# Kernel tuning notes

Measured on AMD Instinct MI355X. Metric: run time of the kernel, lower is better.

## Reference

```python
import jax, jax.numpy as jnp
import numpy as np


def silu(x):
    return x * jax.nn.sigmoid(x)


def conv1x1(x, w, s, b, act):
    # x: [B,Ci,H,W], w: [Co,Ci]; BN folded into per-channel scale s / bias b
    y = jnp.einsum('oi,bihw->bohw', w, x) * s[None, :, None, None] + b[None, :, None, None]
    return silu(y) if act else y


def dwconv3x3(x, w, s, b):
    # depthwise 3x3, groups=C, padding SAME (autopad=1); w: [C,1,3,3]
    y = jax.lax.conv_general_dilated(
        x, w, window_strides=(1, 1), padding=[(1, 1), (1, 1)],
        dimension_numbers=('NCHW', 'OIHW', 'NCHW'),
        feature_group_count=x.shape[1])
    return y * s[None, :, None, None] + b[None, :, None, None]


def attention(x, qkv_w, qkv_s, qkv_b, pe_w, pe_s, pe_b, proj_w, proj_s, proj_b,
              num_heads=4, key_dim=32, head_dim=64):
    B, C, H, W = x.shape
    N = H * W
    scale = key_dim ** -0.5
    qkv = conv1x1(x, qkv_w, qkv_s, qkv_b, act=False)          # [B, C+2*nh*kd, H, W]
    qkv = qkv.reshape(B, num_heads, key_dim * 2 + head_dim, N)
    q = qkv[:, :, :key_dim]                                    # [B,nh,kd,N]
    k = qkv[:, :, key_dim:2 * key_dim]                         # [B,nh,kd,N]
    v = qkv[:, :, 2 * key_dim:]                                # [B,nh,hd,N]
    attn = jnp.einsum('bhdi,bhdj->bhij', q, k) * scale         # [B,nh,N,N]
    attn = jax.nn.softmax(attn, axis=-1)
    out = jnp.einsum('bhdj,bhij->bhdi', v, attn)               # [B,nh,hd,N]
    out = out.reshape(B, C, H, W) + dwconv3x3(v.reshape(B, C, H, W), pe_w, pe_s, pe_b)
    return conv1x1(out, proj_w, proj_s, proj_b, act=False)


def setup_inputs() -> dict:
    key = jax.random.key(0)
    ks = jax.random.split(key, 32)
    B, C1, H, W = 4, 512, 48, 48
    c = C1 // 2  # 256
    h = c + 2 * 32 * 4  # 512
    d = {'x': jax.random.normal(ks[0], (B, C1, H, W), jnp.float32)}
    def w(i, shape):
        return jax.random.normal(ks[i], shape, jnp.float32) * 0.05
    def s(i, n):
        return jax.random.uniform(ks[i], (n,), jnp.float32, 0.5, 1.5)
    def b(i, n):
        return jax.random.normal(ks[i], (n,), jnp.float32) * 0.05
    d['cv1_w'], d['cv1_s'], d['cv1_b'] = w(1, (2 * c, C1)), s(2, 2 * c), b(3, 2 * c)
    d['qkv_w'], d['qkv_s'], d['qkv_b'] = w(4, (h, c)), s(5, h), b(6, h)
    d['pe_w'], d['pe_s'], d['pe_b'] = w(7, (c, 1, 3, 3)), s(8, c), b(9, c)
    d['proj_w'], d['proj_s'], d['proj_b'] = w(10, (c, c)), s(11, c), b(12, c)
    d['ffn1_w'], d['ffn1_s'], d['ffn1_b'] = w(13, (2 * c, c)), s(14, 2 * c), b(15, 2 * c)
    d['ffn2_w'], d['ffn2_s'], d['ffn2_b'] = w(16, (c, 2 * c)), s(17, c), b(18, c)
    d['cv2_w'], d['cv2_s'], d['cv2_b'] = w(19, (C1, 2 * c)), s(20, C1), b(21, C1)
    return d


def reference(x, cv1_w, cv1_s, cv1_b, qkv_w, qkv_s, qkv_b, pe_w, pe_s, pe_b,
              proj_w, proj_s, proj_b, ffn1_w, ffn1_s, ffn1_b, ffn2_w, ffn2_s, ffn2_b,
              cv2_w, cv2_s, cv2_b):
    c = cv1_w.shape[0] // 2  # hidden channels (256)
    ab = conv1x1(x, cv1_w, cv1_s, cv1_b, act=True)
    a, bb = ab[:, :c], ab[:, c:]
    bb = bb + attention(bb, qkv_w, qkv_s, qkv_b, pe_w, pe_s, pe_b,
                        proj_w, proj_s, proj_b)
    f = conv1x1(bb, ffn1_w, ffn1_s, ffn1_b, act=True)
    bb = bb + conv1x1(f, ffn2_w, ffn2_s, ffn2_b, act=False)
    return conv1x1(jnp.concatenate([a, bb], axis=1), cv2_w, cv2_s, cv2_b, act=True)
```

## Files before the change

### kernel.cpp

```cpp
#include <hip/hip_runtime.h>
#include <math.h>

#define N_SP 2304
#define HW 48

typedef unsigned short u16;
typedef short s8v  __attribute__((ext_vector_type(8)));
typedef short s4v  __attribute__((ext_vector_type(4)));
typedef u16   u16x8 __attribute__((ext_vector_type(8)));
typedef float f32x4 __attribute__((ext_vector_type(4)));
typedef unsigned u32x4 __attribute__((ext_vector_type(4)));

__device__ __forceinline__ short f2bf(float x) {
    unsigned u = __float_as_uint(x);
    u += 0x7FFFu + ((u >> 16) & 1u);
    return (short)(u >> 16);
}
__device__ __forceinline__ float bf2f(u16 u) {
    return __uint_as_float((unsigned)u << 16);
}
__device__ __forceinline__ float fexp2(float x) { return __builtin_amdgcn_exp2f(x); }
__device__ __forceinline__ float frcp(float x)  { return __builtin_amdgcn_rcpf(x); }
__device__ __forceinline__ float fsilu(float v) {
    return v * frcp(1.f + fexp2(-1.4426950408889634f * v));
}
__device__ __forceinline__ unsigned cvtpk(float lo, float hi) {
    unsigned r;
    asm("v_cvt_pk_bf16_f32 %0, %1, %2" : "=v"(r) : "v"(lo), "v"(hi));
    return r;
}
__device__ __forceinline__ void gload16(const void* g, void* l) {
    __builtin_amdgcn_global_load_lds(
        (const __attribute__((address_space(1))) void*)g,
        (__attribute__((address_space(3))) void*)l, 16, 0, 0);
}
__device__ __forceinline__ void bar_lgkm() {
    asm volatile("s_waitcnt lgkmcnt(0)" ::: "memory");
    __builtin_amdgcn_s_barrier();
}

__global__ __launch_bounds__(256) void prep(
    const float* __restrict__ X, u16* __restrict__ XT,
    const float* __restrict__ s0, const float* __restrict__ s1,
    const float* __restrict__ s2, const float* __restrict__ s3,
    const float* __restrict__ s4, const float* __restrict__ s5,
    u16* __restrict__ d0, u16* __restrict__ d1, u16* __restrict__ d2,
    u16* __restrict__ d3, u16* __restrict__ d4, u16* __restrict__ d5)
{
    __shared__ float tile[64][65];
    const int t = threadIdx.x;
    if (blockIdx.x < 960) {
        int id = blockIdx.x * 256 + t;
        const int c0 = 65536, c1 = c0 + 32768, c2 = c1 + 16384,
                  c3 = c2 + 32768, c4 = c3 + 32768, c5 = c4 + 65536;
        if (id >= c5) return;
        const float* s; u16* d; int off;
        if      (id < c0) { s = s0; d = d0; off = id; }
        else if (id < c1) { s = s1; d = d1; off = id - c0; }
        else if (id < c2) { s = s2; d = d2; off = id - c1; }
        else if (id < c3) { s = s3; d = d3; off = id - c2; }
        else if (id < c4) { s = s4; d = d4; off = id - c3; }
        else              { s = s5; d = d5; off = id - c4; }
        float4 v = ((const float4*)s)[off];
        s4v p; p[0] = f2bf(v.x); p[1] = f2bf(v.y); p[2] = f2bf(v.z); p[3] = f2bf(v.w);
        ((s4v*)d)[off] = p;
        return;
    }
    const int bid = blockIdx.x - 960;
    const int n0 = (bid % 36) * 64, c0 = ((bid / 36) & 7) * 64, b = bid / 288;
    const float* src = X + (long)b * 512 * N_SP;
    u16* dst = XT + (long)b * N_SP * 512;
    #pragma unroll
    for (int it = 0; it < 16; ++it) {
        int id = t + 256 * it;
        int cl = id >> 6, nl = id & 63;
        tile[cl][nl] = src[(long)(c0 + cl) * N_SP + n0 + nl];
    }
    __syncthreads();
    #pragma unroll
    for (int it = 0; it < 16; ++it) {
        int id = t + 256 * it;
        int nl = id >> 6, cl = id & 63;
        dst[(long)(n0 + nl) * 512 + c0 + cl] = f2bf(tile[cl][nl]);
    }
}

template <int OMODE>
__device__ __forceinline__ void gemm_epilogue(
    float y[4], int nb, int nib, int o, int b_blk, int Mtot,
    const u16* Res, int sR, void* OutP, u16* OutT, int sO)
{
    if (Res) {
        #pragma unroll
        for (int r = 0; r < 4; ++r)
            y[r] += bf2f(Res[(long)(nb + r) * sR + o]);
    }
    if (OMODE == 0) {
        u16* O = (u16*)OutP;
        #pragma unroll
        for (int r = 0; r < 4; ++r)
            O[(long)(nb + r) * sO + o] = (u16)f2bf(y[r]);
    } else if (OMODE == 1 || OMODE == 3) {
        u16* O = (u16*)OutP + (long)b_blk * Mtot * N_SP + (long)o * N_SP + nib;
        s4v pk;
        #pragma unroll
        for (int r = 0; r < 4; ++r) pk[r] = f2bf(y[r]);
        *(s4v*)O = pk;
        if (OMODE == 3) {
            #pragma unroll
            for (int r = 0; r < 4; ++r)
                OutT[(long)(nb + r) * 512 + o] = (u16)f2bf(y[r]);
        }
    } else {
        float* O = (float*)OutP + (long)b_blk * Mtot * N_SP + (long)o * N_SP + nib;
        *(float4*)O = make_float4(y[0], y[1], y[2], y[3]);
    }
}

template <int NO, int OMODE>
__global__ __launch_bounds__(256) void mfma_gemm(
    const u16* __restrict__ A1, const u16* __restrict__ A2, int K1,
    int sA1, int sA2, int K,
    const u16* __restrict__ W,
    const float* __restrict__ S, const float* __restrict__ Bi,
    const u16* __restrict__ Res, int sR,
    void* __restrict__ OutP, u16* __restrict__ OutT, int sO, int Mtot,
    int act)
{
    __shared__ u16 Al[3][64][64];
    __shared__ u16 Bl[3][64][64];
    const int t  = threadIdx.x;
    const int p = blockIdx.x;
    const int cx = p & 7, q = p >> 3;
    const int n0 = (cx * 18 + q / NO) * 64;
    const int o0 = (q % NO) * 64;
    const int lane = t & 63, w = t >> 6;
    const int wn = (w & 1) * 32, wo = (w >> 1) * 32;
    const int li = lane & 15, g = lane >> 4;

    const int b_blk = n0 / N_SP;
    const int n_in0 = n0 - b_blk * N_SP;

    f32x4 acc[2][2];
    #pragma unroll
    for (int fm = 0; fm < 2; ++fm)
        #pragma unroll
        for (int fn = 0; fn < 2; ++fn) acc[fm][fn] = f32x4{0.f, 0.f, 0.f, 0.f};

    auto issue = [&](int buf, int k0) {
        #pragma unroll
        for (int qq = 0; qq < 2; ++qq) {
            int c = t + qq * 256;
            int row = c >> 3;
            int col = ((c & 7) ^ (row & 7)) * 8;
            int kk = k0 + col;
            const u16* ga = (kk < K1) ? (A1 + (long)(n0 + row) * sA1 + kk)
                                      : (A2 + (long)(n0 + row) * sA2 + (kk - K1));
            gload16(ga, (u16*)Al[buf] + (qq * 256 + w * 64) * 8);
            gload16(W + (long)(o0 + row) * K + k0 + col,
                    (u16*)Bl[buf] + (qq * 256 + w * 64) * 8);
        }
    };

    const int NK = K >> 6;
    issue(0, 0);
    if (NK > 1) issue(1, 64);

    for (int ks = 0; ks < NK; ++ks) {
        if (ks + 1 < NK) asm volatile("s_waitcnt vmcnt(4)" ::: "memory");
        else             asm volatile("s_waitcnt vmcnt(0)" ::: "memory");
        __builtin_amdgcn_s_barrier();
        if (ks + 2 < NK) issue((ks + 2) % 3, (ks + 2) << 6);
        const int cur = ks % 3;
        #pragma unroll
        for (int k2 = 0; k2 < 2; ++k2) {
            s8v af[2], bfv[2];
            #pragma unroll
            for (int fm = 0; fm < 2; ++fm) {
                int row = wn + fm * 16 + li;
                af[fm] = *(const s8v*)&Al[cur][row][((g + 4 * k2) ^ (li & 7)) * 8];
            }
            #pragma unroll
            for (int fn = 0; fn < 2; ++fn) {
                int row = wo + fn * 16 + li;
                bfv[fn] = *(const s8v*)&Bl[cur][row][((g + 4 * k2) ^ (li & 7)) * 8];
            }
            #pragma unroll
            for (int fm = 0; fm < 2; ++fm)
                #pragma unroll
                for (int fn = 0; fn < 2; ++fn)
                    acc[fm][fn] = __builtin_amdgcn_mfma_f32_16x16x32_bf16(
                        af[fm], bfv[fn], acc[fm][fn], 0, 0, 0);
        }
    }

    #pragma unroll
    for (int fn = 0; fn < 2; ++fn) {
        const int o = o0 + wo + fn * 16 + li;
        const float sc2 = S[o], bi = Bi[o];
        #pragma unroll
        for (int fm = 0; fm < 2; ++fm) {
            const int nb  = n0 + wn + fm * 16 + 4 * g;
            const int nib = n_in0 + wn + fm * 16 + 4 * g;
            float y[4];
            #pragma unroll
            for (int r = 0; r < 4; ++r) {
                float v = acc[fm][fn][r] * sc2 + bi;
                if (act) v = fsilu(v);
                y[r] = v;
            }
            gemm_epilogue<OMODE>(y, nb, nib, o, b_blk, Mtot, Res, sR, OutP, OutT, sO);
        }
    }
}

template <int NO, int OMODE>
__global__ __launch_bounds__(256) void mfma_gemm_big(
    const u16* __restrict__ A1, const u16* __restrict__ A2, int K1,
    int sA1, int sA2, int K,
    const u16* __restrict__ W,
    const float* __restrict__ S, const float* __restrict__ Bi,
    const u16* __restrict__ Res, int sR,
    void* __restrict__ OutP, u16* __restrict__ OutT, int sO, int Mtot,
    int act)
{
    __shared__ u16 Al[2][128][64];
    __shared__ u16 Bl[2][64][64];
    const int t  = threadIdx.x;
    const int p = blockIdx.x;
    const int cx = p & 7, q = p >> 3;
    const int n0 = (cx * 9 + q / NO) * 128;
    const int o0 = (q % NO) * 64;
    const int lane = t & 63, w = t >> 6;
    const int wn = (w & 1) * 64, wo = (w >> 1) * 32;
    const int li = lane & 15, g = lane >> 4;

    const int b_blk = n0 / N_SP;
    const int n_in0 = n0 - b_blk * N_SP;

    f32x4 acc[4][2];
    #pragma unroll
    for (int fm = 0; fm < 4; ++fm)
        #pragma unroll
        for (int fn = 0; fn < 2; ++fn) acc[fm][fn] = f32x4{0.f, 0.f, 0.f, 0.f};

    auto issue = [&](int buf, int k0) {
        #pragma unroll
        for (int qq = 0; qq < 4; ++qq) {
            int c = t + qq * 256;
            int row = c >> 3;
            int col = ((c & 7) ^ (row & 7)) * 8;
            int kk = k0 + col;
            const u16* ga = (kk < K1) ? (A1 + (long)(n0 + row) * sA1 + kk)
                                      : (A2 + (long)(n0 + row) * sA2 + (kk - K1));
            gload16(ga, (u16*)Al[buf] + (qq * 256 + w * 64) * 8);
        }
        #pragma unroll
        for (int qq = 0; qq < 2; ++qq) {
            int c = t + qq * 256;
            int row = c >> 3;
            int col = ((c & 7) ^ (row & 7)) * 8;
            gload16(W + (long)(o0 + row) * K + k0 + col,
                    (u16*)Bl[buf] + (qq * 256 + w * 64) * 8);
        }
    };

    const int NK = K >> 6;
    issue(0, 0);
    asm volatile("s_waitcnt vmcnt(0)" ::: "memory");
    __builtin_amdgcn_s_barrier();

    int cur = 0;
    for (int ks = 0; ks < NK; ++ks) {
        if (ks + 1 < NK) issue(cur ^ 1, (ks + 1) << 6);
        #pragma unroll
        for (int k2 = 0; k2 < 2; ++k2) {
            s8v af[4], bfv[2];
            #pragma unroll
            for (int fm = 0; fm < 4; ++fm) {
                int row = wn + fm * 16 + li;
                af[fm] = *(const s8v*)&Al[cur][row][((g + 4 * k2) ^ (li & 7)) * 8];
            }
            #pragma unroll
            for (int fn = 0; fn < 2; ++fn) {
                int row = wo + fn * 16 + li;
                bfv[fn] = *(const s8v*)&Bl[cur][row][((g + 4 * k2) ^ (li & 7)) * 8];
            }
            #pragma unroll
            for (int fm = 0; fm < 4; ++fm)
                #pragma unroll
                for (int fn = 0; fn < 2; ++fn)
                    acc[fm][fn] = __builtin_amdgcn_mfma_f32_16x16x32_bf16(
                        af[fm], bfv[fn], acc[fm][fn], 0, 0, 0);
        }
        if (ks + 1 < NK) {
            asm volatile("s_waitcnt vmcnt(0)" ::: "memory");
            __builtin_amdgcn_s_barrier();
        }
        cur ^= 1;
    }

    #pragma unroll
    for (int fn = 0; fn < 2; ++fn) {
        const int o = o0 + wo + fn * 16 + li;
        const float sc2 = S[o], bi = Bi[o];
        #pragma unroll
        for (int fm = 0; fm < 4; ++fm) {
            const int nb  = n0 + wn + fm * 16 + 4 * g;
            const int nib = n_in0 + wn + fm * 16 + 4 * g;
            float y[4];
            #pragma unroll
            for (int r = 0; r < 4; ++r) {
                float v = acc[fm][fn][r] * sc2 + bi;
                if (act) v = fsilu(v);
                y[r] = v;
            }
            gemm_epilogue<OMODE>(y, nb, nib, o, b_blk, Mtot, Res, sR, OutP, OutT, sO);
        }
    }
}

__global__ __launch_bounds__(256) void attn_mfma(const u16* __restrict__ qkv,
    const u16* __restrict__ qkvT,
    u16* __restrict__ Opart, float* __restrict__ mpart, float* __restrict__ lpart)
{
    const int N = N_SP;
    __shared__ u16 Klds[2][64][40];
    __shared__ u16 Vlds[2][64][72];

    const int p = blockIdx.x;
    const int cx = p & 7, q = p >> 3;
    const int i0 = (q % 18) * 128;
    const int bhz = cx + 8 * (q / 18);
    const int bh = bhz & 15, z = bhz >> 4;
    const int b = bh >> 2, h = bh & 3;
    const int t = threadIdx.x;
    const int w = t >> 6;
    const int lane = t & 63;
    const int li = lane & 15;
    const int g  = lane >> 4;
    const float qscale = 0.17677669529663687f * 1.4426950408889634f;

    const u16* qp  = qkv  + ((long)b * 512 + (long)h * 128) * N;
    const u16* vp  = qp + 64L * N;
    const u16* qTp = qkvT + (long)b * N * 512 + h * 128;

    const int ia = i0 + w * 16 + li;
    const int ib = ia + 64;

    s8v qf[2];
    {
        s8v qa = *(const s8v*)(qTp + (long)ia * 512 + 8 * g);
        s8v qb = *(const s8v*)(qTp + (long)ib * 512 + 8 * g);
        #pragma unroll
        for (int r = 0; r < 8; ++r) {
            qf[0][r] = f2bf(bf2f((u16)qa[r]) * qscale);
            qf[1][r] = f2bf(bf2f((u16)qb[r]) * qscale);
        }
    }

    f32x4 oacc[2][4];
    #pragma unroll
    for (int q2 = 0; q2 < 2; ++q2)
        #pragma unroll
        for (int dt = 0; dt < 4; ++dt) oacc[q2][dt] = f32x4{0.f, 0.f, 0.f, 0.f};
    float m_run[2] = {-1e30f, -1e30f}, l_run[2] = {0.f, 0.f};

    const int kj2 = t & 63;
    const int kd  = (t >> 6) * 8;
    const int vd  = t >> 2;
    const int vjb = (t & 3) * 16;

    const int jbase = z * 576;
    u16x8 kr, vr0, vr1;
    auto ldregs = [&](int j0) {
        kr  = *(const u16x8*)(qTp + (long)(j0 + kj2) * 512 + 32 + kd);
        vr0 = *(const u16x8*)(vp + (long)vd * N + j0 + vjb);
        vr1 = *(const u16x8*)(vp + (long)vd * N + j0 + vjb + 8);
    };

    ldregs(jbase);
    *(u16x8*)&Klds[0][kj2][kd]     = kr;
    *(u16x8*)&Vlds[0][vd][vjb]     = vr0;
    *(u16x8*)&Vlds[0][vd][vjb + 8] = vr1;
    ldregs(jbase + 64);
    bar_lgkm();

    int cur = 0;
    for (int it = 0; it < 9; ++it) {
        if (it + 1 < 9) {
            *(u16x8*)&Klds[cur ^ 1][kj2][kd]     = kr;
            *(u16x8*)&Vlds[cur ^ 1][vd][vjb]     = vr0;
            *(u16x8*)&Vlds[cur ^ 1][vd][vjb + 8] = vr1;
            if (it + 2 < 9) ldregs(jbase + (it + 2) * 64);
        }

        f32x4 sacc[2][4];
        __builtin_amdgcn_s_setprio(1);
        #pragma unroll
        for (int js = 0; js < 4; ++js) {
            s8v kf = *(const s8v*)&Klds[cur][js * 16 + li][8 * g];
            f32x4 zz = f32x4{0.f, 0.f, 0.f, 0.f};
            sacc[0][js] = __builtin_amdgcn_mfma_f32_16x16x32_bf16(kf, qf[0], zz, 0, 0, 0);
            sacc[1][js] = __builtin_amdgcn_mfma_f32_16x16x32_bf16(kf, qf[1], zz, 0, 0, 0);
        }
        __builtin_amdgcn_s_setprio(0);

        #pragma unroll
        for (int q2 = 0; q2 < 2; ++q2) {
            float tm = -1e30f;
            #pragma unroll
            for (int js = 0; js < 4; ++js)
                #pragma unroll
                for (int r = 0; r < 4; ++r) tm = fmaxf(tm, sacc[q2][js][r]);
            tm = fmaxf(tm, __shfl_xor(tm, 16, 64));
            tm = fmaxf(tm, __shfl_xor(tm, 32, 64));
            if (__any(tm > m_run[q2] + 8.f)) {
                float mnew = fmaxf(m_run[q2], tm);
                float scl  = fexp2(m_run[q2] - mnew);
                l_run[q2] *= scl;
                #pragma unroll
                for (int dt = 0; dt < 4; ++dt) oacc[q2][dt] *= scl;
                m_run[q2] = mnew;
            }
            float ts = 0.f;
            #pragma unroll
            for (int js = 0; js < 4; ++js)
                #pragma unroll
                for (int r = 0; r < 4; ++r) {
                    float pv = fexp2(sacc[q2][js][r] - m_run[q2]);
                    sacc[q2][js][r] = pv;
                    ts += pv;
                }
            ts += __shfl_xor(ts, 16, 64);
            ts += __shfl_xor(ts, 32, 64);
            l_run[q2] += ts;
        }

        __builtin_amdgcn_s_setprio(1);
        #pragma unroll
        for (int ks = 0; ks < 2; ++ks) {
            s8v pf[2];
            #pragma unroll
            for (int q2 = 0; q2 < 2; ++q2) {
                u32x4 pw;
                pw[0] = cvtpk(sacc[q2][2 * ks][0],     sacc[q2][2 * ks][1]);
                pw[1] = cvtpk(sacc[q2][2 * ks][2],     sacc[q2][2 * ks][3]);
                pw[2] = cvtpk(sacc[q2][2 * ks + 1][0], sacc[q2][2 * ks + 1][1]);
                pw[3] = cvtpk(sacc[q2][2 * ks + 1][2], sacc[q2][2 * ks + 1][3]);
                pf[q2] = __builtin_bit_cast(s8v, pw);
            }
            #pragma unroll
            for (int dt = 0; dt < 4; ++dt) {
                int d = dt * 16 + li;
                s4v lo = *(const s4v*)&Vlds[cur][d][32 * ks + 4 * g];
                s4v hi = *(const s4v*)&Vlds[cur][d][32 * ks + 16 + 4 * g];
                s8v vf = __builtin_shufflevector(lo, hi, 0, 1, 2, 3, 4, 5, 6, 7);
                oacc[0][dt] = __builtin_amdgcn_mfma_f32_16x16x32_bf16(vf, pf[0], oacc[0][dt], 0, 0, 0);
                oacc[1][dt] = __builtin_amdgcn_mfma_f32_16x16x32_bf16(vf, pf[1], oacc[1][dt], 0, 0, 0);
            }
        }
        __builtin_amdgcn_s_setprio(0);

        if (it + 1 < 9) bar_lgkm();
        cur ^= 1;
    }

    const long cb = (long)(z * 16 + bh);
    #pragma unroll
    for (int q2 = 0; q2 < 2; ++q2) {
        const int i = q2 ? ib : ia;
        #pragma unroll
        for (int dt = 0; dt < 4; ++dt)
            #pragma unroll
            for (int r = 0; r < 4; ++r)
                Opart[(cb * 64 + dt * 16 + 4 * g + r) * N + i] = (u16)f2bf(oacc[q2][dt][r]);
        if (g == 0) {
            mpart[cb * N + i] = m_run[q2];
            lpart[cb * N + i] = l_run[q2];
        }
    }
}

__global__ __launch_bounds__(256) void attn_combine(
    const u16* __restrict__ Opart, const float* __restrict__ mpart,
    const float* __restrict__ lpart, const u16* __restrict__ qkvT,
    const float* __restrict__ pw, const float* __restrict__ ps,
    const float* __restrict__ pb, u16* __restrict__ attnT)
{
    const int N = N_SP;
    const int i0 = blockIdx.x * 64;
    const int bh = blockIdx.y;
    const int b = bh >> 2, h = bh & 3;
    const int t = threadIdx.x;
    const int il = t & 63, dq = t >> 6;
    const int d0 = dq * 16;
    const int i = i0 + il;

    float mm[4], ll[4];
    #pragma unroll
    for (int c = 0; c < 4; ++c) {
        mm[c] = mpart[((long)(c * 16 + bh)) * N + i];
        ll[c] = lpart[((long)(c * 16 + bh)) * N + i];
    }
    float ms = fmaxf(fmaxf(mm[0], mm[1]), fmaxf(mm[2], mm[3]));
    float wc[4], lsum = 0.f;
    #pragma unroll
    for (int c = 0; c < 4; ++c) {
        wc[c] = fexp2(mm[c] - ms);
        lsum += wc[c] * ll[c];
    }
    float inv = frcp(lsum);

    const int y = i / HW, x = i - (i / HW) * HW;
    const u16* vT = qkvT + (long)b * N * 512 + h * 128 + 64 + d0;
    float pe[16];
    #pragma unroll
    for (int dd = 0; dd < 16; ++dd) pe[dd] = 0.f;
    #pragma unroll
    for (int dy = -1; dy <= 1; ++dy) {
        int yy = y + dy;
        if (yy < 0 || yy >= HW) continue;
        #pragma unroll
        for (int dx = -1; dx <= 1; ++dx) {
            int xx = x + dx;
            if (xx < 0 || xx >= HW) continue;
            const int k = (dy + 1) * 3 + (dx + 1);
            const u16* pvt = vT + (long)(yy * HW + xx) * 512;
            u16x8 a0 = *(const u16x8*)pvt;
            u16x8 a1 = *(const u16x8*)(pvt + 8);
            #pragma unroll
            for (int dd = 0; dd < 8; ++dd) {
                pe[dd]     += pw[(h * 64 + d0 + dd) * 9 + k]     * bf2f((u16)a0[dd]);
                pe[8 + dd] += pw[(h * 64 + d0 + 8 + dd) * 9 + k] * bf2f((u16)a1[dd]);
            }
        }
    }

    u16 ob[16];
    #pragma unroll
    for (int dd = 0; dd < 16; ++dd) {
        const int d = d0 + dd;
        const int cg = h * 64 + d;
        float o = 0.f;
        #pragma unroll
        for (int c = 0; c < 4; ++c)
            o += wc[c] * bf2f(Opart[((long)(c * 16 + bh) * 64 + d) * N + i]);
        o = o * inv + pe[dd] * ps[cg] + pb[cg];
        ob[dd] = (u16)f2bf(o);
    }
    u16* dst = attnT + ((long)b * N + i) * 256 + h * 64 + d0;
    *(u16x8*)dst       = *(u16x8*)&ob[0];
    *(u16x8*)(dst + 8) = *(u16x8*)&ob[8];
}

extern "C" void kernel_launch(void* const* d_in, const int* in_sizes, int n_in,
                              void* d_out, int out_size, void* d_ws, size_t ws_size,
                              hipStream_t stream)
{
    const long N = N_SP;
    const float* x      = (const float*)d_in[0];
    const float* cv1_w  = (const float*)d_in[1];
    const float* cv1_s  = (const float*)d_in[2];
    const float* cv1_b  = (const float*)d_in[3];
    const float* qkv_w  = (const float*)d_in[4];
    const float* qkv_s  = (const float*)d_in[5];
    const float* qkv_b  = (const float*)d_in[6];
    const float* pe_w   = (const float*)d_in[7];
    const float* pe_s   = (const float*)d_in[8];
    const float* pe_b   = (const float*)d_in[9];
    const float* proj_w = (const float*)d_in[10];
    const float* proj_s = (const float*)d_in[11];
    const float* proj_b = (const float*)d_in[12];
    const float* ffn1_w = (const float*)d_in[13];
    const float* ffn1_s = (const float*)d_in[14];
    const float* ffn1_b = (const float*)d_in[15];
    const float* ffn2_w = (const float*)d_in[16];
    const float* ffn2_s = (const float*)d_in[17];
    const float* ffn2_b = (const float*)d_in[18];
    const float* cv2_w  = (const float*)d_in[19];
    const float* cv2_s  = (const float*)d_in[20];
    const float* cv2_b  = (const float*)d_in[21];
    float* out = (float*)d_out;

    u16* ws = (u16*)d_ws;
    u16* xT      = ws;
    u16* abT     = xT      + 4L * N * 512;
    u16* qkvb    = abT     + 4L * N * 512;
    u16* qkvT    = qkvb    + 4L * N * 512;
    u16* attnT   = qkvT    + 4L * N * 512;
    u16* bb2T    = attnT   + 4L * N * 256;
    u16* fT      = bb2T    + 4L * N * 256;
    u16* bb3T    = fT      + 4L * N * 512;
    u16* w_cv1   = bb3T    + 4L * N * 256;
    u16* w_qkv   = w_cv1   + 512L * 512;
    u16* w_proj  = w_qkv   + 512L * 256;
    u16* w_ffn1  = w_proj  + 256L * 256;
    u16* w_ffn2  = w_ffn1  + 512L * 256;
    u16* w_cv2   = w_ffn2  + 256L * 512;
    u16* Opart   = w_cv2   + 512L * 512;
    float* mpart = (float*)(Opart + 4L * 16 * 64 * N);
    float* lpart = mpart + 4L * 16 * N;

    dim3 blk(256);
    const int BIGK = 1 << 28;

    prep<<<2112, blk, 0, stream>>>(x, xT,
        cv1_w, qkv_w, proj_w, ffn1_w, ffn2_w, cv2_w,
        w_cv1, w_qkv, w_proj, w_ffn1, w_ffn2, w_cv2);

    mfma_gemm_big<8, 0><<<576, blk, 0, stream>>>(
        xT, nullptr, BIGK, 512, 0, 512, w_cv1, cv1_s, cv1_b,
        nullptr, 0, abT, nullptr, 512, 512, 1);

    mfma_gemm_big<8, 3><<<576, blk, 0, stream>>>(
        abT + 256, nullptr, BIGK, 512, 0, 256, w_qkv, qkv_s, qkv_b,
        nullptr, 0, qkvb, qkvT, 0, 512, 0);

    attn_mfma<<<1152, blk, 0, stream>>>(qkvb, qkvT, Opart, mpart, lpart);

    attn_combine<<<dim3(36, 16), blk, 0, stream>>>(
        Opart, mpart, lpart, qkvT, pe_w, pe_s, pe_b, attnT);

    mfma_gemm<4, 0><<<576, blk, 0, stream>>>(
        attnT, nullptr, BIGK, 256, 0, 256, w_proj, proj_s, proj_b,
        abT + 256, 512, bb2T, nullptr, 256, 256, 0);

    mfma_gemm_big<8, 0><<<576, blk, 0, stream>>>(
        bb2T, nullptr, BIGK, 256, 0, 256, w_ffn1, ffn1_s, ffn1_b,
        nullptr, 0, fT, nullptr, 512, 512, 1);

    mfma_gemm<4, 0><<<576, blk, 0, stream>>>(
        fT, nullptr, BIGK, 512, 0, 512, w_ffn2, ffn2_s, ffn2_b,
        bb2T, 256, bb3T, nullptr, 256, 256, 0);

    mfma_gemm_big<8, 2><<<576, blk, 0, stream>>>(
        abT, bb3T, 256, 512, 256, 512, w_cv2, cv2_s, cv2_b,
        nullptr, 0, out, nullptr, 0, 512, 1);
}
```

Baseline: 125.6 us.

## Fuse attention combine and depthwise PE into proj GEMM kernel

Merges the split-softmax combine plus depthwise positional conv with the projection 1x1 GEMM and residual add in one kernel. Each block computes a 32-pixel x 256-channel attention tile into LDS, then runs MFMA against double-buffered proj weight slices. This removes the attnT round trip through global memory and one kernel launch. The cost is a grid of only 288 blocks with heavier per-thread register use (32 pe accumulators), which may lower occupancy and parallelism compared with the previous 576-block launches.

```diff
diff --git a/kernel.cpp b/kernel.cpp
--- a/kernel.cpp
+++ b/kernel.cpp
@@ -482,76 +482,155 @@
     }
 }
 
-__global__ __launch_bounds__(256) void attn_combine(
+__global__ __launch_bounds__(256) void combine_proj(
     const u16* __restrict__ Opart, const float* __restrict__ mpart,
     const float* __restrict__ lpart, const u16* __restrict__ qkvT,
     const float* __restrict__ pw, const float* __restrict__ ps,
-    const float* __restrict__ pb, u16* __restrict__ attnT)
+    const float* __restrict__ pb,
+    const u16* __restrict__ Wp, const float* __restrict__ S,
+    const float* __restrict__ Bi, const u16* __restrict__ abT,
+    u16* __restrict__ bb2T)
 {
     const int N = N_SP;
-    const int i0 = blockIdx.x * 64;
-    const int bh = blockIdx.y;
-    const int b = bh >> 2, h = bh & 3;
-    const int t = threadIdx.x;
-    const int il = t & 63, dq = t >> 6;
-    const int d0 = dq * 16;
-    const int i = i0 + il;
-
-    float mm[4], ll[4];
-    #pragma unroll
-    for (int c = 0; c < 4; ++c) {
-        mm[c] = mpart[((long)(c * 16 + bh)) * N + i];
-        ll[c] = lpart[((long)(c * 16 + bh)) * N + i];
-    }
-    float ms = fmaxf(fmaxf(mm[0], mm[1]), fmaxf(mm[2], mm[3]));
-    float wc[4], lsum = 0.f;
-    #pragma unroll
-    for (int c = 0; c < 4; ++c) {
-        wc[c] = fexp2(mm[c] - ms);
-        lsum += wc[c] * ll[c];
-    }
-    float inv = frcp(lsum);
-
-    const int y = i / HW, x = i - (i / HW) * HW;
-    const u16* vT = qkvT + (long)b * N * 512 + h * 128 + 64 + d0;
-    float pe[16];
-    #pragma unroll
-    for (int dd = 0; dd < 16; ++dd) pe[dd] = 0.f;
-    #pragma unroll
-    for (int dy = -1; dy <= 1; ++dy) {
-        int yy = y + dy;
-        if (yy < 0 || yy >= HW) continue;
-        #pragma unroll
-        for (int dx = -1; dx <= 1; ++dx) {
-            int xx = x + dx;
-            if (xx < 0 || xx >= HW) continue;
-            const int k = (dy + 1) * 3 + (dx + 1);
-            const u16* pvt = vT + (long)(yy * HW + xx) * 512;
-            u16x8 a0 = *(const u16x8*)pvt;
-            u16x8 a1 = *(const u16x8*)(pvt + 8);
+    __shared__ u16 At[8][32][40];
+    __shared__ u16 Wl[2][256][32];
+
+    const int bid = blockIdx.x;
+    const int i0 = (bid % 72) * 32;
+    const int b  = bid / 72;
+    const int t  = threadIdx.x;
+    const int lane = t & 63, w = t >> 6;
+    const int li = lane & 15, g = lane >> 4;
+
+    auto issueW = [&](int buf, int ks) {
+        #pragma unroll
+        for (int qq = 0; qq < 4; ++qq) {
+            int idx = qq * 256 + t;
+            int row = idx >> 2, c = idx & 3;
+            gload16(Wp + (long)row * 256 + ks * 32 + ((c ^ (row & 3)) * 8),
+                    (u16*)Wl[buf] + (qq * 256 + w * 64) * 8);
+        }
+    };
+    issueW(0, 0);
+
+    {
+        const int il  = t & 31;
+        const int grp = t >> 5;
+        const int i   = i0 + il;
+        const int h   = grp >> 1;
+        const int d0  = (grp & 1) * 32;
+        const int bh  = b * 4 + h;
+
+        float mm[4], ll[4];
+        #pragma unroll
+        for (int c = 0; c < 4; ++c) {
+            mm[c] = mpart[((long)(c * 16 + bh)) * N + i];
+            ll[c] = lpart[((long)(c * 16 + bh)) * N + i];
+        }
+        float ms = fmaxf(fmaxf(mm[0], mm[1]), fmaxf(mm[2], mm[3]));
+        float wc[4], lsum = 0.f;
+        #pragma unroll
+        for (int c = 0; c < 4; ++c) {
+            wc[c] = fexp2(mm[c] - ms);
+            lsum += wc[c] * ll[c];
+        }
+        float inv = frcp(lsum);
+
+        const int y = i / HW, x = i - (i / HW) * HW;
+        const u16* vT = qkvT + (long)b * N * 512 + h * 128 + 64 + d0;
+        float pe[32];
+        #pragma unroll
+        for (int dd = 0; dd < 32; ++dd) pe[dd] = 0.f;
+        #pragma unroll
+        for (int dy = -1; dy <= 1; ++dy) {
+            int yy = y + dy;
+            if (yy < 0 || yy >= HW) continue;
+            #pragma unroll
+            for (int dx = -1; dx <= 1; ++dx) {
+                int xx = x + dx;
+                if (xx < 0 || xx >= HW) continue;
+                const int k = (dy + 1) * 3 + (dx + 1);
+                const u16* pvt = vT + (long)(yy * HW + xx) * 512;
+                #pragma unroll
+                for (int v8 = 0; v8 < 4; ++v8) {
+                    u16x8 a = *(const u16x8*)(pvt + v8 * 8);
+                    #pragma unroll
+                    for (int dd = 0; dd < 8; ++dd)
+                        pe[v8 * 8 + dd] +=
+                            pw[(h * 64 + d0 + v8 * 8 + dd) * 9 + k] * bf2f((u16)a[dd]);
+                }
+            }
+        }
+
+        #pragma unroll
+        for (int c8 = 0; c8 < 4; ++c8) {
+            u16x8 outv;
             #pragma unroll
             for (int dd = 0; dd < 8; ++dd) {
-                pe[dd]     += pw[(h * 64 + d0 + dd) * 9 + k]     * bf2f((u16)a0[dd]);
-                pe[8 + dd] += pw[(h * 64 + d0 + 8 + dd) * 9 + k] * bf2f((u16)a1[dd]);
-            }
-        }
-    }
-
-    u16 ob[16];
-    #pragma unroll
-    for (int dd = 0; dd < 16; ++dd) {
-        const int d = d0 + dd;
-        const int cg = h * 64 + d;
-        float o = 0.f;
-        #pragma unroll
-        for (int c = 0; c < 4; ++c)
-            o += wc[c] * bf2f(Opart[((long)(c * 16 + bh) * 64 + d) * N + i]);
-        o = o * inv + pe[dd] * ps[cg] + pb[cg];
-        ob[dd] = (u16)f2bf(o);
-    }
-    u16* dst = attnT + ((long)b * N + i) * 256 + h * 64 + d0;
-    *(u16x8*)dst       = *(u16x8*)&ob[0];
-    *(u16x8*)(dst + 8) = *(u16x8*)&ob[8];
+                const int d  = d0 + c8 * 8 + dd;
+                const int cg = h * 64 + d;
+                float o = 0.f;
+                #pragma unroll
+                for (int c = 0; c < 4; ++c)
+                    o += wc[c] * bf2f(Opart[((long)(c * 16 + bh) * 64 + d) * N + i]);
+                o = o * inv + pe[c8 * 8 + dd] * ps[cg] + pb[cg];
+                outv[dd] = (u16)f2bf(o);
+            }
+            *(u16x8*)&At[grp][il][(c8 ^ (il & 3)) * 8] = outv;
+        }
+    }
+
+    asm volatile("s_waitcnt vmcnt(0)" ::: "memory");
+    __syncthreads();
+    const int wo = w * 64;
+    f32x4 acc[2][4];
+    #pragma unroll
+    for (int fm = 0; fm < 2; ++fm)
+        #pragma unroll
+        for (int fn = 0; fn < 4; ++fn) acc[fm][fn] = f32x4{0.f, 0.f, 0.f, 0.f};
+
+    for (int ks = 0; ks < 8; ++ks) {
+        if (ks + 1 < 8) issueW((ks + 1) & 1, ks + 1);
+        const int cur = ks & 1;
+        s8v af[2], bfv[4];
+        #pragma unroll
+        for (int fm = 0; fm < 2; ++fm) {
+            int row = fm * 16 + li;
+            af[fm] = *(const s8v*)&At[ks][row][(g ^ (row & 3)) * 8];
+        }
+        #pragma unroll
+        for (int fn = 0; fn < 4; ++fn) {
+            int row = wo + fn * 16 + li;
+            bfv[fn] = *(const s8v*)&Wl[cur][row][(g ^ (row & 3)) * 8];
+        }
+        #pragma unroll
+        for (int fm = 0; fm < 2; ++fm)
+            #pragma unroll
+            for (int fn = 0; fn < 4; ++fn)
+                acc[fm][fn] = __builtin_amdgcn_mfma_f32_16x16x32_bf16(
+                    af[fm], bfv[fn], acc[fm][fn], 0, 0, 0);
+        if (ks + 1 < 8) {
+            asm volatile("s_waitcnt vmcnt(0)" ::: "memory");
+            __builtin_amdgcn_s_barrier();
+        }
+    }
+
+    #pragma unroll
+    for (int fn = 0; fn < 4; ++fn) {
+        const int o = wo + fn * 16 + li;
+        const float sc2 = S[o], bi = Bi[o];
+        #pragma unroll
+        for (int fm = 0; fm < 2; ++fm) {
+            const int nl = fm * 16 + 4 * g;
+            const long nglob = (long)b * N + i0 + nl;
+            #pragma unroll
+            for (int r = 0; r < 4; ++r) {
+                float v = acc[fm][fn][r] * sc2 + bi
+                        + bf2f(abT[(nglob + r) * 512 + 256 + o]);
+                bb2T[(nglob + r) * 256 + o] = (u16)f2bf(v);
+            }
+        }
+    }
 }
 
 extern "C" void kernel_launch(void* const* d_in, const int* in_sizes, int n_in,
@@ -588,8 +667,7 @@
     u16* abT     = xT      + 4L * N * 512;
     u16* qkvb    = abT     + 4L * N * 512;
     u16* qkvT    = qkvb    + 4L * N * 512;
-    u16* attnT   = qkvT    + 4L * N * 512;
-    u16* bb2T    = attnT   + 4L * N * 256;
+    u16* bb2T    = qkvT    + 4L * N * 512;
     u16* fT      = bb2T    + 4L * N * 256;
     u16* bb3T    = fT      + 4L * N * 512;
     u16* w_cv1   = bb3T    + 4L * N * 256;
@@ -619,12 +697,9 @@
 
     attn_mfma<<<1152, blk, 0, stream>>>(qkvb, qkvT, Opart, mpart, lpart);
 
-    attn_combine<<<dim3(36, 16), blk, 0, stream>>>(
-        Opart, mpart, lpart, qkvT, pe_w, pe_s, pe_b, attnT);
-
-    mfma_gemm<4, 0><<<576, blk, 0, stream>>>(
-        attnT, nullptr, BIGK, 256, 0, 256, w_proj, proj_s, proj_b,
-        abT + 256, 512, bb2T, nullptr, 256, 256, 0);
+    combine_proj<<<288, blk, 0, stream>>>(
+        Opart, mpart, lpart, qkvT, pe_w, pe_s, pe_b,
+        w_proj, proj_s, proj_b, abT, bb2T);
 
     mfma_gemm_big<8, 0><<<576, blk, 0, stream>>>(
         bb2T, nullptr, BIGK, 256, 0, 256, w_ffn1, ffn1_s, ffn1_b,
```

New measurement: 144.4 us. +15.0%, slower.
